# Optimization experiments

Hardware: AMD Instinct MI355X
Metric: run time of the kernel (lower is better)

## Reference

```python
import jax, jax.numpy as jnp
import numpy as np

N, T, H, W, C = 64, 32, 64, 64, 256
HID, NB, P, OUT = 512, 12, 7, 388
CIN = P * P + 2  # 49 patch values + 2 normalized coords


def _ln(x, s):
    # haiku LayerNorm(axis=-1, create_scale=True, create_offset=False), eps=1e-5
    m = jnp.mean(x, axis=-1, keepdims=True)
    v = jnp.var(x, axis=-1, keepdims=True)
    return (x - m) * jax.lax.rsqrt(v + 1e-5) * s


def _dwconv(x, w, b, groups):
    # hk.DepthwiseConv1D, NWC, stride 1, SAME padding; w: [K, 1, C_out]
    y = jax.lax.conv_general_dilated(
        x, w, (1,), 'SAME', dimension_numbers=('NWC', 'WIO', 'NWC'),
        feature_group_count=groups)
    return y + b


def _forward(feature_grid, query_feats, pos, in_w, in_b, dw1_w, dw1_b, dw2_w,
             dw2_b, ln1_s, ln2_s, up_w, up_b, down_w, down_b, lnf_s, out_w,
             out_b):
    pad = P - 1
    # cost volume: einsum('bnc,bthwc->tbnhw') with batch=1, laid out [N,T,H,W]
    corrs = jnp.einsum('nc,thwc->nthw', query_feats, feature_grid)
    padded = jnp.pad(corrs, ((0, 0), (0, 0), (pad, pad), (pad, pad)))
    # extract_patch_depthwise_conv: the separable bilinear bump kernel convolved
    # VALID over the padded map equals a bilinear sample at (o + pos + P/2 - 1).
    pp = pos + P / 2.0 - 1.0  # [N,T,2] (y,x)
    iy = jnp.floor(pp[..., 0])
    ix = jnp.floor(pp[..., 1])
    fy = (pp[..., 0] - iy)[..., None, None]
    fx = (pp[..., 1] - ix)[..., None, None]
    offs = jnp.arange(P, dtype=jnp.int32)
    y0 = iy.astype(jnp.int32)[..., None] + offs  # [N,T,P]
    x0 = ix.astype(jnp.int32)[..., None] + offs  # [N,T,P]
    gat = jax.vmap(jax.vmap(lambda img, yi, xi: img[yi][:, xi]))
    patch = ((1 - fy) * (1 - fx) * gat(padded, y0, x0)
             + (1 - fy) * fx * gat(padded, y0, x0 + 1)
             + fy * (1 - fx) * gat(padded, y0 + 1, x0)
             + fy * fx * gat(padded, y0 + 1, x0 + 1))  # [N,T,P,P]
    x = jnp.concatenate(
        [patch.reshape(patch.shape[0], patch.shape[1], P * P),
         pos / jnp.float32(H)], axis=-1)  # [N,T,CIN]
    # PIPSMLPMixer
    x = x @ in_w + in_b  # [N,T,HID]
    for i in range(NB):
        # PIPsConvBlock: depthwise_conv_residual
        skip = x
        h = _ln(x, ln1_s[i])
        h = jax.nn.gelu(_dwconv(h, dw1_w[i], dw1_b[i], HID))  # ch mult 4
        h = _dwconv(h, dw2_w[i], dw2_b[i], HID * 4)           # ch mult 1
        h = h[..., 0::4] + h[..., 1::4] + h[..., 2::4] + h[..., 3::4]
        x = h + skip
        # conv_channels_mixer
        skip = x
        h = _ln(x, ln2_s[i])
        h = jax.nn.gelu(h @ up_w[i] + up_b[i]) @ down_w[i] + down_b[i]
        x = h + skip
    x = _ln(x, lnf_s)
    return x @ out_w + out_b  # [N,T,OUT]


def setup_inputs() -> dict:
    key = jax.random.key(0)
    ks = jax.random.split(key, 12)
    s = 0.02
    return dict(
        feature_grid=jax.random.normal(ks[0], (T, H, W, C), jnp.float32),
        query_feats=jax.random.normal(ks[1], (N, C), jnp.float32),
        pos=jax.random.uniform(ks[2], (N, T, 2), jnp.float32) * (H - 8),
        in_w=jax.random.normal(ks[3], (CIN, HID), jnp.float32) * s,
        in_b=jnp.zeros((HID,), jnp.float32),
        dw1_w=jax.random.normal(ks[4], (NB, 3, 1, HID * 4), jnp.float32) * s,
        dw1_b=jnp.zeros((NB, HID * 4), jnp.float32),
        dw2_w=jax.random.normal(ks[5], (NB, 3, 1, HID * 4), jnp.float32) * s,
        dw2_b=jnp.zeros((NB, HID * 4), jnp.float32),
        ln1_s=jnp.ones((NB, HID), jnp.float32),
        ln2_s=jnp.ones((NB, HID), jnp.float32),
        up_w=jax.random.normal(ks[6], (NB, HID, HID * 4), jnp.float32) * s,
        up_b=jnp.zeros((NB, HID * 4), jnp.float32),
        down_w=jax.random.normal(ks[7], (NB, HID * 4, HID), jnp.float32) * s,
        down_b=jnp.zeros((NB, HID), jnp.float32),
        lnf_s=jnp.ones((HID,), jnp.float32),
        out_w=jax.random.normal(ks[8], (HID, OUT), jnp.float32) * s,
        out_b=jnp.zeros((OUT,), jnp.float32),
    )


def reference(feature_grid, query_feats, pos, in_w, in_b, dw1_w, dw1_b, dw2_w,
              dw2_b, ln1_s, ln2_s, up_w, up_b, down_w, down_b, lnf_s, out_w,
              out_b):
    return _forward(feature_grid, query_feats, pos, in_w, in_b, dw1_w, dw1_b,
                    dw2_w, dw2_b, ln1_s, ln2_s, up_w, up_b, down_w, down_b,
                    lnf_s, out_w, out_b)
```

## Files before the change

kernel.cpp:

```cpp
#include <hip/hip_runtime.h>
#include <hip/hip_bf16.h>

#define N_    64
#define T_    32
#define H_    64
#define W_    64
#define C_    256
#define HID   512
#define HID4  2048
#define NBLK  12
#define P_    7
#define OUT_  388
#define OUTP  448
#define CIN   51
#define M_    (N_*T_)

typedef __attribute__((ext_vector_type(4))) float f32x4;
typedef __attribute__((ext_vector_type(8))) short bf16x8;

__device__ __forceinline__ float gelu_f(float x) {
    float x3 = x * x * x;
    return 0.5f * x * (1.f + tanhf(0.7978845608028654f * (x + 0.044715f * x3)));
}

__device__ __forceinline__ void gload_lds16(const void* g, void* l) {
    __builtin_amdgcn_global_load_lds(
        (const __attribute__((address_space(1))) void*)g,
        (__attribute__((address_space(3))) void*)l, 16, 0, 0);
}

__global__ __launch_bounds__(256) void patch_kernel(
    const float* __restrict__ fg, const float* __restrict__ qf,
    const float* __restrict__ pos, const float* __restrict__ in_w,
    const float* __restrict__ in_b, float* __restrict__ x) {
    __shared__ float4 q[64];
    __shared__ float g[8][8];
    __shared__ float xrow[CIN];
    int m = blockIdx.x;
    int n = m >> 5;
    int t = m & (T_ - 1);
    int tid = threadIdx.x, wid = tid >> 6, lane = tid & 63;
    if (tid < 64) q[tid] = *(const float4*)&qf[n * C_ + tid * 4];
    __syncthreads();
    float posy = pos[m * 2 + 0];
    float posx = pos[m * 2 + 1];
    float py = posy + 2.5f;
    float px = posx + 2.5f;
    int iy = (int)floorf(py), ix = (int)floorf(px);
    float fy = py - (float)iy, fx = px - (float)ix;
    float4 qv = q[lane];
    #pragma unroll
    for (int i = 0; i < 16; ++i) {
        int idx = wid * 16 + i;
        int a = idx >> 3, b = idx & 7;
        int y = iy + a - 6, xc = ix + b - 6;
        float partial = 0.f;
        if (y >= 0 && y < H_ && xc >= 0 && xc < W_) {
            const float4* fp = (const float4*)&fg[(((t * H_ + y) * W_) + xc) * C_];
            float4 v = fp[lane];
            partial = v.x * qv.x + v.y * qv.y + v.z * qv.z + v.w * qv.w;
        }
        #pragma unroll
        for (int o2 = 32; o2; o2 >>= 1) partial += __shfl_xor(partial, o2);
        if (lane == 0) g[a][b] = partial;
    }
    __syncthreads();
    if (tid < 49) {
        int p = tid / 7, qq = tid % 7;
        xrow[tid] = (1.f - fy) * (1.f - fx) * g[p][qq]
                  + (1.f - fy) * fx         * g[p][qq + 1]
                  + fy         * (1.f - fx) * g[p + 1][qq]
                  + fy         * fx         * g[p + 1][qq + 1];
    } else if (tid == 49) {
        xrow[49] = posy * (1.f / 64.f);
    } else if (tid == 50) {
        xrow[50] = posx * (1.f / 64.f);
    }
    __syncthreads();
    float acc0 = in_b[tid], acc1 = in_b[tid + 256];
    #pragma unroll
    for (int c = 0; c < CIN; ++c) {
        float rv = xrow[c];
        acc0 += rv * in_w[c * HID + tid];
        acc1 += rv * in_w[c * HID + tid + 256];
    }
    x[m * HID + tid] = acc0;
    x[m * HID + tid + 256] = acc1;
}

__global__ __launch_bounds__(512) void fused_dw_kernel(
    const float* __restrict__ xin, float* __restrict__ xout,
    __hip_bfloat16* __restrict__ t1b,
    const float* __restrict__ ln1s, const float* __restrict__ ln2s,
    const float* __restrict__ w1, const float* __restrict__ b1,
    const float* __restrict__ w2, const float* __restrict__ b2) {
    __shared__ float2 part[12][8];
    int n = blockIdx.y;
    int t0 = blockIdx.x * 8;
    int j = threadIdx.x;
    int lane = j & 63, wave = j >> 6;

    float xv[12];
    #pragma unroll
    for (int tt = 0; tt < 12; ++tt) {
        int t = t0 - 2 + tt;
        xv[tt] = (t >= 0 && t < T_) ? xin[(n * T_ + t) * HID + j] : 0.f;
    }
    #pragma unroll
    for (int tt = 0; tt < 12; ++tt) {
        float s = xv[tt], q = xv[tt] * xv[tt];
        #pragma unroll
        for (int o = 32; o; o >>= 1) { s += __shfl_xor(s, o); q += __shfl_xor(q, o); }
        if (lane == 0) part[tt][wave] = make_float2(s, q);
    }
    __syncthreads();
    float s1v = ln1s[j];
    float xl[12];
    #pragma unroll
    for (int tt = 0; tt < 12; ++tt) {
        int t = t0 - 2 + tt;
        if (t >= 0 && t < T_) {
            float s = 0.f, q = 0.f;
            #pragma unroll
            for (int w = 0; w < 8; ++w) { float2 p = part[tt][w]; s += p.x; q += p.y; }
            float mean = s * (1.f / HID);
            float var  = q * (1.f / HID) - mean * mean;
            xl[tt] = (xv[tt] - mean) * rsqrtf(var + 1e-5f) * s1v;
        } else xl[tt] = 0.f;
    }
    float w1a[12], w2a[12], b1a[4];
    #pragma unroll
    for (int r = 0; r < 3; ++r) {
        *(float4*)&w1a[r * 4] = *(const float4*)&w1[r * HID4 + 4 * j];
        *(float4*)&w2a[r * 4] = *(const float4*)&w2[r * HID4 + 4 * j];
    }
    *(float4*)&b1a[0] = *(const float4*)&b1[4 * j];
    float4 b2v = *(const float4*)&b2[4 * j];
    float h[8];
    float b2sum = b2v.x + b2v.y + b2v.z + b2v.w;
    #pragma unroll
    for (int i = 0; i < 8; ++i) h[i] = b2sum;
    #pragma unroll
    for (int k = 0; k < 4; ++k) {
        float gk[10];
        #pragma unroll
        for (int idx = 0; idx < 10; ++idx) {
            int tp = t0 - 1 + idx;
            if (tp >= 0 && tp < T_) {
                float a = b1a[k] + w1a[0 * 4 + k] * xl[idx]
                                 + w1a[1 * 4 + k] * xl[idx + 1]
                                 + w1a[2 * 4 + k] * xl[idx + 2];
                gk[idx] = gelu_f(a);
            } else gk[idx] = 0.f;
        }
        #pragma unroll
        for (int i = 0; i < 8; ++i)
            h[i] += w2a[0 * 4 + k] * gk[i] + w2a[1 * 4 + k] * gk[i + 1]
                  + w2a[2 * 4 + k] * gk[i + 2];
    }
    float xn[8];
    #pragma unroll
    for (int i = 0; i < 8; ++i) xn[i] = xv[i + 2] + h[i];
    __syncthreads();
    #pragma unroll
    for (int i = 0; i < 8; ++i) {
        float s = xn[i], q = xn[i] * xn[i];
        #pragma unroll
        for (int o = 32; o; o >>= 1) { s += __shfl_xor(s, o); q += __shfl_xor(q, o); }
        if (lane == 0) part[i][wave] = make_float2(s, q);
    }
    __syncthreads();
    float s2v = ln2s[j];
    #pragma unroll
    for (int i = 0; i < 8; ++i) {
        float s = 0.f, q = 0.f;
        #pragma unroll
        for (int w = 0; w < 8; ++w) { float2 p = part[i][w]; s += p.x; q += p.y; }
        float mean = s * (1.f / HID);
        float var  = q * (1.f / HID) - mean * mean;
        float rstd = rsqrtf(var + 1e-5f);
        int m = (n * T_ + t0 + i) * HID + j;
        xout[m] = xn[i];
        t1b[m] = __float2bfloat16((xn[i] - mean) * rstd * s2v);
    }
}

__global__ __launch_bounds__(256) void ln_kernel(
    const float* __restrict__ in, const float* __restrict__ s,
    __hip_bfloat16* __restrict__ outb) {
    int wid = threadIdx.x >> 6, lane = threadIdx.x & 63;
    int row = blockIdx.x * 4 + wid;
    const float* r = in + row * HID + lane * 8;
    float4 v0 = *(const float4*)r;
    float4 v1 = *(const float4*)(r + 4);
    float sum = v0.x + v0.y + v0.z + v0.w + v1.x + v1.y + v1.z + v1.w;
    float sq  = v0.x*v0.x + v0.y*v0.y + v0.z*v0.z + v0.w*v0.w
              + v1.x*v1.x + v1.y*v1.y + v1.z*v1.z + v1.w*v1.w;
    #pragma unroll
    for (int o = 32; o; o >>= 1) { sum += __shfl_xor(sum, o); sq += __shfl_xor(sq, o); }
    float mean = sum * (1.f / HID);
    float var  = sq * (1.f / HID) - mean * mean;
    float rstd = rsqrtf(var + 1e-5f);
    const float* sp = s + lane * 8;
    float4 s0 = *(const float4*)sp;
    float4 s1 = *(const float4*)(sp + 4);
    float o[8];
    o[0] = (v0.x - mean) * rstd * s0.x; o[1] = (v0.y - mean) * rstd * s0.y;
    o[2] = (v0.z - mean) * rstd * s0.z; o[3] = (v0.w - mean) * rstd * s0.w;
    o[4] = (v1.x - mean) * rstd * s1.x; o[5] = (v1.y - mean) * rstd * s1.y;
    o[6] = (v1.z - mean) * rstd * s1.z; o[7] = (v1.w - mean) * rstd * s1.w;
    alignas(16) __hip_bfloat16 tmp[8];
    #pragma unroll
    for (int i = 0; i < 8; ++i) tmp[i] = __float2bfloat16(o[i]);
    *(bf16x8*)&outb[row * HID + lane * 8] = *(bf16x8*)tmp;
}

__global__ __launch_bounds__(256) void tcvt_kernel(
    const float* __restrict__ src, __hip_bfloat16* __restrict__ dst,
    int R, int C, int Cpad) {
    __shared__ float tile[32][33];
    size_t zb = blockIdx.z;
    src += zb * (size_t)R * C;
    dst += zb * (size_t)Cpad * R;
    int c0 = blockIdx.x * 32, r0 = blockIdx.y * 32;
    int tx = threadIdx.x & 31, ty = threadIdx.x >> 5;
    #pragma unroll
    for (int i = 0; i < 4; ++i) {
        int r = r0 + ty + i * 8, c = c0 + tx;
        tile[ty + i * 8][tx] = (c < C) ? src[(size_t)r * C + c] : 0.f;
    }
    __syncthreads();
    #pragma unroll
    for (int i = 0; i < 4; ++i) {
        int c = c0 + ty + i * 8, r = r0 + tx;
        dst[(size_t)c * R + r] = __float2bfloat16(tile[tx][ty + i * 8]);
    }
}

template <int KG, int EPI>
__global__ __launch_bounds__(256 * KG) void gemm64(
    const __hip_bfloat16* __restrict__ A, const __hip_bfloat16* __restrict__ Bt,
    const float* __restrict__ bias, float* __restrict__ Cf,
    __hip_bfloat16* __restrict__ Cb, int K, int ldN, int Nstore) {
    __shared__ alignas(16) __hip_bfloat16 As[KG][2][64 * 64];
    __shared__ alignas(16) __hip_bfloat16 Bs[KG][2][64 * 64];
    int tid = threadIdx.x;
    int lane = tid & 63, wave = tid >> 6;
    int g = wave >> 2;
    int w4 = wave & 3;
    int wr = w4 >> 1, wc = w4 & 1;
    int row0 = blockIdx.y * 64, col0 = blockIdx.x * 64;
    int Kg = K / KG;
    int kbase = g * Kg;

    f32x4 acc[2][2];
    #pragma unroll
    for (int m = 0; m < 2; ++m)
        #pragma unroll
        for (int n = 0; n < 2; ++n)
            acc[m][n] = (f32x4){0.f, 0.f, 0.f, 0.f};

    int rI = lane >> 3;
    int cp = lane & 7;

    auto stage = [&](int buf, int k0) {
        #pragma unroll
        for (int s = 0; s < 2; ++s) {
            int rbase = w4 * 16 + s * 8;
            int row = rbase + rI;
            int corig = cp ^ (row & 7);
            gload_lds16(A + (size_t)(row0 + row) * K + kbase + k0 + corig * 8,
                        (char*)As[g][buf] + rbase * 128);
        }
        #pragma unroll
        for (int s = 0; s < 2; ++s) {
            int rbase = w4 * 16 + s * 8;
            int row = rbase + rI;
            int corig = cp ^ (row & 7);
            gload_lds16(Bt + (size_t)(col0 + row) * K + kbase + k0 + corig * 8,
                        (char*)Bs[g][buf] + rbase * 128);
        }
    };

    int nsteps = Kg >> 6;
    stage(0, 0);
    for (int step = 0; step < nsteps; ++step) {
        int cur = step & 1;
        __builtin_amdgcn_s_barrier();
        if (step + 1 < nsteps) {
            stage(cur ^ 1, (step + 1) * 64);
            asm volatile("s_waitcnt vmcnt(4)" ::: "memory");
        } else {
            asm volatile("s_waitcnt vmcnt(0)" ::: "memory");
        }
        __builtin_amdgcn_sched_barrier(0);
        __builtin_amdgcn_s_barrier();
        __builtin_amdgcn_sched_barrier(0);
        #pragma unroll
        for (int kk = 0; kk < 2; ++kk) {
            bf16x8 af[2], bfr[2];
            #pragma unroll
            for (int m = 0; m < 2; ++m) {
                int row = wr * 32 + m * 16 + (lane & 15);
                int chunk = (kk * 4 + (lane >> 4)) ^ (row & 7);
                af[m] = *(const bf16x8*)((const char*)As[g][cur] + row * 128 + chunk * 16);
            }
            #pragma unroll
            for (int n = 0; n < 2; ++n) {
                int row = wc * 32 + n * 16 + (lane & 15);
                int chunk = (kk * 4 + (lane >> 4)) ^ (row & 7);
                bfr[n] = *(const bf16x8*)((const char*)Bs[g][cur] + row * 128 + chunk * 16);
            }
            __builtin_amdgcn_s_setprio(1);
            #pragma unroll
            for (int m = 0; m < 2; ++m)
                #pragma unroll
                for (int n = 0; n < 2; ++n)
                    acc[m][n] = __builtin_amdgcn_mfma_f32_16x16x32_bf16(
                        af[m], bfr[n], acc[m][n], 0, 0, 0);
            __builtin_amdgcn_s_setprio(0);
        }
    }

    int cr = (lane >> 4) * 4;
    int cc = lane & 15;

    if (KG == 2) {
        float* scratch = (float*)&As[0][0][0];
        __syncthreads();
        if (g == 1) {
            #pragma unroll
            for (int m = 0; m < 2; ++m)
                #pragma unroll
                for (int n = 0; n < 2; ++n)
                    #pragma unroll
                    for (int j = 0; j < 4; ++j)
                        scratch[(wr * 32 + m * 16 + cr + j) * 64 +
                                wc * 32 + n * 16 + cc] = acc[m][n][j];
        }
        __syncthreads();
        if (g == 1) return;
        #pragma unroll
        for (int m = 0; m < 2; ++m)
            #pragma unroll
            for (int n = 0; n < 2; ++n)
                #pragma unroll
                for (int j = 0; j < 4; ++j)
                    acc[m][n][j] += scratch[(wr * 32 + m * 16 + cr + j) * 64 +
                                            wc * 32 + n * 16 + cc];
    }

    #pragma unroll
    for (int m = 0; m < 2; ++m) {
        #pragma unroll
        for (int n = 0; n < 2; ++n) {
            #pragma unroll
            for (int j = 0; j < 4; ++j) {
                int row = row0 + wr * 32 + m * 16 + cr + j;
                int col = col0 + wc * 32 + n * 16 + cc;
                float v = acc[m][n][j];
                if (EPI == 0) {
                    if (col < Nstore)
                        Cf[(size_t)row * Nstore + col] = v + bias[col];
                } else if (EPI == 1) {
                    v = gelu_f(v + bias[col]);
                    Cb[(size_t)row * ldN + col] = __float2bfloat16(v);
                } else {
                    Cf[(size_t)row * ldN + col] += v + bias[col];
                }
            }
        }
    }
}

extern "C" void kernel_launch(void* const* d_in, const int* in_sizes, int n_in,
                              void* d_out, int out_size, void* d_ws, size_t ws_size,
                              hipStream_t stream) {
    const float* fg     = (const float*)d_in[0];
    const float* qf     = (const float*)d_in[1];
    const float* pos    = (const float*)d_in[2];
    const float* in_w   = (const float*)d_in[3];
    const float* in_b   = (const float*)d_in[4];
    const float* dw1_w  = (const float*)d_in[5];
    const float* dw1_b  = (const float*)d_in[6];
    const float* dw2_w  = (const float*)d_in[7];
    const float* dw2_b  = (const float*)d_in[8];
    const float* ln1_s  = (const float*)d_in[9];
    const float* ln2_s  = (const float*)d_in[10];
    const float* up_w   = (const float*)d_in[11];
    const float* up_b   = (const float*)d_in[12];
    const float* down_w = (const float*)d_in[13];
    const float* down_b = (const float*)d_in[14];
    const float* lnf_s  = (const float*)d_in[15];
    const float* out_w  = (const float*)d_in[16];
    const float* out_b  = (const float*)d_in[17];
    float* out = (float*)d_out;

    char* ws = (char*)d_ws;
    float* xa = (float*)ws;                        ws += (size_t)M_ * HID * 4;
    float* xb = (float*)ws;                        ws += (size_t)M_ * HID * 4;
    __hip_bfloat16* t1b = (__hip_bfloat16*)ws;     ws += (size_t)M_ * HID * 2;
    __hip_bfloat16* t2b = (__hip_bfloat16*)ws;     ws += (size_t)M_ * HID4 * 2;
    __hip_bfloat16* upT  = (__hip_bfloat16*)ws;    ws += (size_t)NBLK * HID4 * HID * 2;
    __hip_bfloat16* dnT  = (__hip_bfloat16*)ws;    ws += (size_t)NBLK * HID * HID4 * 2;
    __hip_bfloat16* outT = (__hip_bfloat16*)ws;    ws += (size_t)OUTP * HID * 2;

    tcvt_kernel<<<dim3(HID4 / 32, HID / 32, NBLK), 256, 0, stream>>>(
        up_w, upT, HID, HID4, HID4);
    tcvt_kernel<<<dim3(HID / 32, HID4 / 32, NBLK), 256, 0, stream>>>(
        down_w, dnT, HID4, HID, HID);
    tcvt_kernel<<<dim3(OUTP / 32, HID / 32, 1), 256, 0, stream>>>(
        out_w, outT, HID, OUT_, OUTP);

    patch_kernel<<<M_, 256, 0, stream>>>(fg, qf, pos, in_w, in_b, xa);

    float* xc = xa;
    float* xn = xb;
    for (int b = 0; b < NBLK; ++b) {
        fused_dw_kernel<<<dim3(4, N_), 512, 0, stream>>>(
            xc, xn, t1b, ln1_s + b * HID, ln2_s + b * HID,
            dw1_w + b * 3 * HID4, dw1_b + b * HID4,
            dw2_w + b * 3 * HID4, dw2_b + b * HID4);
        gemm64<1, 1><<<dim3(HID4 / 64, M_ / 64), 256, 0, stream>>>(
            t1b, upT + (size_t)b * HID4 * HID, up_b + b * HID4, nullptr, t2b,
            HID, HID4, HID4);
        gemm64<2, 2><<<dim3(HID / 64, M_ / 64), 512, 0, stream>>>(
            t2b, dnT + (size_t)b * HID * HID4, down_b + b * HID, xn, nullptr,
            HID4, HID, HID);
        float* tmp = xc; xc = xn; xn = tmp;
    }

    ln_kernel<<<M_ / 4, 256, 0, stream>>>(xc, lnf_s, t1b);
    gemm64<1, 0><<<dim3(OUTP / 64, M_ / 64), 256, 0, stream>>>(
        t1b, outT, out_b, out, nullptr, HID, OUT_, OUT_);
}
```

Before: 640.3 us.

## Template GEMM tile sizes, use 128x128 tiles for up-projection, add block swizzle

Generalizes the GEMM kernel over block tile and per-wave fragment counts, then launches the up-projection with 128x128 tiles and the output projection with 128x64 tiles. Larger tiles raise MFMA work per shared-memory load and cut global reloads of A and B. The kernel also remaps block IDs in strides of eight to change scheduling order and cache locality. The risk is fewer workgroups: the up GEMM drops to 256 blocks, which may underfill the 256-CU device, and the larger register footprint could lower occupancy.

```diff
diff --git a/kernel.cpp b/kernel.cpp
--- a/kernel.cpp
+++ b/kernel.cpp
@@ -237,27 +237,35 @@
     }
 }
 
-template <int KG, int EPI>
-__global__ __launch_bounds__(256 * KG) void gemm64(
+template <int BM, int BN, int FM, int FN, int KG, int EPI>
+__global__ __launch_bounds__(256 * KG) void gemm_tile(
     const __hip_bfloat16* __restrict__ A, const __hip_bfloat16* __restrict__ Bt,
     const float* __restrict__ bias, float* __restrict__ Cf,
     __hip_bfloat16* __restrict__ Cb, int K, int ldN, int Nstore) {
-    __shared__ alignas(16) __hip_bfloat16 As[KG][2][64 * 64];
-    __shared__ alignas(16) __hip_bfloat16 Bs[KG][2][64 * 64];
+    constexpr int LOADS = (BM + BN) / 32;
+    __shared__ alignas(16) __hip_bfloat16 As[KG][2][BM * 64];
+    __shared__ alignas(16) __hip_bfloat16 Bs[KG][2][BN * 64];
     int tid = threadIdx.x;
     int lane = tid & 63, wave = tid >> 6;
     int g = wave >> 2;
     int w4 = wave & 3;
     int wr = w4 >> 1, wc = w4 & 1;
-    int row0 = blockIdx.y * 64, col0 = blockIdx.x * 64;
+
+    int gx = gridDim.x;
+    int nwg = gx * gridDim.y;
+    int bid = blockIdx.y * gx + blockIdx.x;
+    int cpx = nwg >> 3;
+    int wg = (bid & 7) * cpx + (bid >> 3);
+    int row0 = (wg / gx) * BM, col0 = (wg % gx) * BN;
+
     int Kg = K / KG;
     int kbase = g * Kg;
 
-    f32x4 acc[2][2];
-    #pragma unroll
-    for (int m = 0; m < 2; ++m)
-        #pragma unroll
-        for (int n = 0; n < 2; ++n)
+    f32x4 acc[FM][FN];
+    #pragma unroll
+    for (int m = 0; m < FM; ++m)
+        #pragma unroll
+        for (int n = 0; n < FN; ++n)
             acc[m][n] = (f32x4){0.f, 0.f, 0.f, 0.f};
 
     int rI = lane >> 3;
@@ -265,16 +273,16 @@
 
     auto stage = [&](int buf, int k0) {
         #pragma unroll
-        for (int s = 0; s < 2; ++s) {
-            int rbase = w4 * 16 + s * 8;
+        for (int s = 0; s < BM / 32; ++s) {
+            int rbase = w4 * (BM / 4) + s * 8;
             int row = rbase + rI;
             int corig = cp ^ (row & 7);
             gload_lds16(A + (size_t)(row0 + row) * K + kbase + k0 + corig * 8,
                         (char*)As[g][buf] + rbase * 128);
         }
         #pragma unroll
-        for (int s = 0; s < 2; ++s) {
-            int rbase = w4 * 16 + s * 8;
+        for (int s = 0; s < BN / 32; ++s) {
+            int rbase = w4 * (BN / 4) + s * 8;
             int row = rbase + rI;
             int corig = cp ^ (row & 7);
             gload_lds16(Bt + (size_t)(col0 + row) * K + kbase + k0 + corig * 8,
@@ -289,7 +297,7 @@
         __builtin_amdgcn_s_barrier();
         if (step + 1 < nsteps) {
             stage(cur ^ 1, (step + 1) * 64);
-            asm volatile("s_waitcnt vmcnt(4)" ::: "memory");
+            asm volatile("s_waitcnt vmcnt(%0)" :: "n"(LOADS) : "memory");
         } else {
             asm volatile("s_waitcnt vmcnt(0)" ::: "memory");
         }
@@ -298,24 +306,24 @@
         __builtin_amdgcn_sched_barrier(0);
         #pragma unroll
         for (int kk = 0; kk < 2; ++kk) {
-            bf16x8 af[2], bfr[2];
-            #pragma unroll
-            for (int m = 0; m < 2; ++m) {
-                int row = wr * 32 + m * 16 + (lane & 15);
+            bf16x8 af[FM], bfr[FN];
+            #pragma unroll
+            for (int m = 0; m < FM; ++m) {
+                int row = wr * FM * 16 + m * 16 + (lane & 15);
                 int chunk = (kk * 4 + (lane >> 4)) ^ (row & 7);
                 af[m] = *(const bf16x8*)((const char*)As[g][cur] + row * 128 + chunk * 16);
             }
             #pragma unroll
-            for (int n = 0; n < 2; ++n) {
-                int row = wc * 32 + n * 16 + (lane & 15);
+            for (int n = 0; n < FN; ++n) {
+                int row = wc * FN * 16 + n * 16 + (lane & 15);
                 int chunk = (kk * 4 + (lane >> 4)) ^ (row & 7);
                 bfr[n] = *(const bf16x8*)((const char*)Bs[g][cur] + row * 128 + chunk * 16);
             }
             __builtin_amdgcn_s_setprio(1);
             #pragma unroll
-            for (int m = 0; m < 2; ++m)
+            for (int m = 0; m < FM; ++m)
                 #pragma unroll
-                for (int n = 0; n < 2; ++n)
+                for (int n = 0; n < FN; ++n)
                     acc[m][n] = __builtin_amdgcn_mfma_f32_16x16x32_bf16(
                         af[m], bfr[n], acc[m][n], 0, 0, 0);
             __builtin_amdgcn_s_setprio(0);
@@ -330,34 +338,34 @@
         __syncthreads();
         if (g == 1) {
             #pragma unroll
-            for (int m = 0; m < 2; ++m)
+            for (int m = 0; m < FM; ++m)
                 #pragma unroll
-                for (int n = 0; n < 2; ++n)
+                for (int n = 0; n < FN; ++n)
                     #pragma unroll
                     for (int j = 0; j < 4; ++j)
-                        scratch[(wr * 32 + m * 16 + cr + j) * 64 +
-                                wc * 32 + n * 16 + cc] = acc[m][n][j];
+                        scratch[(wr * FM * 16 + m * 16 + cr + j) * BN +
+                                wc * FN * 16 + n * 16 + cc] = acc[m][n][j];
         }
         __syncthreads();
         if (g == 1) return;
         #pragma unroll
-        for (int m = 0; m < 2; ++m)
-            #pragma unroll
-            for (int n = 0; n < 2; ++n)
+        for (int m = 0; m < FM; ++m)
+            #pragma unroll
+            for (int n = 0; n < FN; ++n)
                 #pragma unroll
                 for (int j = 0; j < 4; ++j)
-                    acc[m][n][j] += scratch[(wr * 32 + m * 16 + cr + j) * 64 +
-                                            wc * 32 + n * 16 + cc];
-    }
-
-    #pragma unroll
-    for (int m = 0; m < 2; ++m) {
-        #pragma unroll
-        for (int n = 0; n < 2; ++n) {
+                    acc[m][n][j] += scratch[(wr * FM * 16 + m * 16 + cr + j) * BN +
+                                            wc * FN * 16 + n * 16 + cc];
+    }
+
+    #pragma unroll
+    for (int m = 0; m < FM; ++m) {
+        #pragma unroll
+        for (int n = 0; n < FN; ++n) {
             #pragma unroll
             for (int j = 0; j < 4; ++j) {
-                int row = row0 + wr * 32 + m * 16 + cr + j;
-                int col = col0 + wc * 32 + n * 16 + cc;
+                int row = row0 + wr * FM * 16 + m * 16 + cr + j;
+                int col = col0 + wc * FN * 16 + n * 16 + cc;
                 float v = acc[m][n][j];
                 if (EPI == 0) {
                     if (col < Nstore)
@@ -421,16 +429,16 @@
             xc, xn, t1b, ln1_s + b * HID, ln2_s + b * HID,
             dw1_w + b * 3 * HID4, dw1_b + b * HID4,
             dw2_w + b * 3 * HID4, dw2_b + b * HID4);
-        gemm64<1, 1><<<dim3(HID4 / 64, M_ / 64), 256, 0, stream>>>(
+        gemm_tile<128, 128, 4, 4, 1, 1><<<dim3(HID4 / 128, M_ / 128), 256, 0, stream>>>(
             t1b, upT + (size_t)b * HID4 * HID, up_b + b * HID4, nullptr, t2b,
             HID, HID4, HID4);
-        gemm64<2, 2><<<dim3(HID / 64, M_ / 64), 512, 0, stream>>>(
+        gemm_tile<64, 64, 2, 2, 2, 2><<<dim3(HID / 64, M_ / 64), 512, 0, stream>>>(
             t2b, dnT + (size_t)b * HID * HID4, down_b + b * HID, xn, nullptr,
             HID4, HID, HID);
         float* tmp = xc; xc = xn; xn = tmp;
     }
 
     ln_kernel<<<M_ / 4, 256, 0, stream>>>(xc, lnf_s, t1b);
-    gemm64<1, 0><<<dim3(OUTP / 64, M_ / 64), 256, 0, stream>>>(
+    gemm_tile<128, 64, 4, 2, 1, 0><<<dim3(OUTP / 64, M_ / 128), 256, 0, stream>>>(
         t1b, outT, out_b, out, nullptr, HID, OUT_, OUT_);
 }
```

Result: slower. 695.9 us (+8.7%).

## Hold A operand in registers for K=512 GEMMs with MFMA-friendly transposed layout

Applied to the files above, without the earlier changes.

The LN outputs are now written in a chunked-transposed bf16 layout (8-element column groups by row) so each wave can load its 16 A rows for the whole K=512 directly into registers. A new gemm_regA kernel stages only B through LDS, with each wave computing a 16x64 tile, and is used for the up-projection and final output GEMMs. The up and down GEMMs also get an XCD-aware block swizzle to improve L2 locality. The cost is 16 extra bf16x8 registers per thread and scattered 2-byte stores from fused_dw_kernel into the transposed layout, which may be poorly coalesced.

```diff
diff --git a/kernel.cpp b/kernel.cpp
--- a/kernel.cpp
+++ b/kernel.cpp
@@ -90,7 +90,7 @@
 
 __global__ __launch_bounds__(512) void fused_dw_kernel(
     const float* __restrict__ xin, float* __restrict__ xout,
-    __hip_bfloat16* __restrict__ t1b,
+    __hip_bfloat16* __restrict__ t1T,
     const float* __restrict__ ln1s, const float* __restrict__ ln2s,
     const float* __restrict__ w1, const float* __restrict__ b1,
     const float* __restrict__ w2, const float* __restrict__ b2) {
@@ -171,6 +171,7 @@
     }
     __syncthreads();
     float s2v = ln2s[j];
+    int cbase = j >> 3, csub = j & 7;
     #pragma unroll
     for (int i = 0; i < 8; ++i) {
         float s = 0.f, q = 0.f;
@@ -179,15 +180,16 @@
         float mean = s * (1.f / HID);
         float var  = q * (1.f / HID) - mean * mean;
         float rstd = rsqrtf(var + 1e-5f);
-        int m = (n * T_ + t0 + i) * HID + j;
-        xout[m] = xn[i];
-        t1b[m] = __float2bfloat16((xn[i] - mean) * rstd * s2v);
+        int row = n * T_ + t0 + i;
+        xout[row * HID + j] = xn[i];
+        t1T[((size_t)cbase * M_ + row) * 8 + csub] =
+            __float2bfloat16((xn[i] - mean) * rstd * s2v);
     }
 }
 
 __global__ __launch_bounds__(256) void ln_kernel(
     const float* __restrict__ in, const float* __restrict__ s,
-    __hip_bfloat16* __restrict__ outb) {
+    __hip_bfloat16* __restrict__ t1T) {
     int wid = threadIdx.x >> 6, lane = threadIdx.x & 63;
     int row = blockIdx.x * 4 + wid;
     const float* r = in + row * HID + lane * 8;
@@ -212,7 +214,7 @@
     alignas(16) __hip_bfloat16 tmp[8];
     #pragma unroll
     for (int i = 0; i < 8; ++i) tmp[i] = __float2bfloat16(o[i]);
-    *(bf16x8*)&outb[row * HID + lane * 8] = *(bf16x8*)tmp;
+    *(bf16x8*)&t1T[((size_t)lane * M_ + row) * 8] = *(bf16x8*)tmp;
 }
 
 __global__ __launch_bounds__(256) void tcvt_kernel(
@@ -237,20 +239,128 @@
     }
 }
 
-template <int KG, int EPI>
-__global__ __launch_bounds__(256 * KG) void gemm64(
+template <int EPI, int SWZ>
+__global__ __launch_bounds__(256, 4) void gemm_regA(
+    const __hip_bfloat16* __restrict__ At,
+    const __hip_bfloat16* __restrict__ Bt,
+    const float* __restrict__ bias, float* __restrict__ Cf,
+    __hip_bfloat16* __restrict__ Cb, int ldN, int Nstore) {
+    constexpr int K = 512;
+    __shared__ alignas(16) __hip_bfloat16 Bs[2][64 * 64];
+    int tid = threadIdx.x;
+    int lane = tid & 63, w = tid >> 6;
+
+    int row0, col0;
+    if (SWZ) {
+        int bid = blockIdx.y * gridDim.x + blockIdx.x;
+        int chunk = gridDim.y >> 3;
+        int xcd = bid & 7;
+        int i = bid >> 3;
+        row0 = (xcd * chunk + (i % chunk)) * 64;
+        col0 = (i / chunk) * 64;
+    } else {
+        row0 = blockIdx.y * 64;
+        col0 = blockIdx.x * 64;
+    }
+
+    int sub = lane >> 4;
+    int arow = row0 + w * 16 + (lane & 15);
+    bf16x8 areg[16];
+    #pragma unroll
+    for (int kb = 0; kb < 16; ++kb) {
+        int c = kb * 4 + sub;
+        areg[kb] = *(const bf16x8*)&At[((size_t)c * M_ + arow) * 8];
+    }
+
+    int rI = lane >> 3;
+    int cp = lane & 7;
+    auto stageB = [&](int buf, int k0) {
+        #pragma unroll
+        for (int s = 0; s < 2; ++s) {
+            int rbase = w * 16 + s * 8;
+            int row = rbase + rI;
+            int corig = cp ^ (row & 7);
+            gload_lds16(Bt + (size_t)(col0 + row) * K + k0 + corig * 8,
+                        (char*)Bs[buf] + rbase * 128);
+        }
+    };
+
+    f32x4 acc[4];
+    #pragma unroll
+    for (int n = 0; n < 4; ++n) acc[n] = (f32x4){0.f, 0.f, 0.f, 0.f};
+
+    stageB(0, 0);
+    #pragma unroll
+    for (int step = 0; step < 8; ++step) {
+        int cur = step & 1;
+        __builtin_amdgcn_s_barrier();
+        if (step < 7) {
+            stageB(cur ^ 1, (step + 1) * 64);
+            asm volatile("s_waitcnt vmcnt(2)" ::: "memory");
+        } else {
+            asm volatile("s_waitcnt vmcnt(0)" ::: "memory");
+        }
+        __builtin_amdgcn_sched_barrier(0);
+        __builtin_amdgcn_s_barrier();
+        __builtin_amdgcn_sched_barrier(0);
+        #pragma unroll
+        for (int kk = 0; kk < 2; ++kk) {
+            bf16x8 bfr[4];
+            #pragma unroll
+            for (int n = 0; n < 4; ++n) {
+                int row = n * 16 + (lane & 15);
+                int chunk = (kk * 4 + sub) ^ (row & 7);
+                bfr[n] = *(const bf16x8*)((const char*)Bs[cur] + row * 128 + chunk * 16);
+            }
+            __builtin_amdgcn_s_setprio(1);
+            #pragma unroll
+            for (int n = 0; n < 4; ++n)
+                acc[n] = __builtin_amdgcn_mfma_f32_16x16x32_bf16(
+                    areg[step * 2 + kk], bfr[n], acc[n], 0, 0, 0);
+            __builtin_amdgcn_s_setprio(0);
+        }
+    }
+
+    int cr = (lane >> 4) * 4;
+    int cc = lane & 15;
+    #pragma unroll
+    for (int n = 0; n < 4; ++n) {
+        #pragma unroll
+        for (int j = 0; j < 4; ++j) {
+            int row = row0 + w * 16 + cr + j;
+            int col = col0 + n * 16 + cc;
+            float v = acc[n][j];
+            if (EPI == 0) {
+                if (col < Nstore)
+                    Cf[(size_t)row * Nstore + col] = v + bias[col];
+            } else {
+                v = gelu_f(v + bias[col]);
+                Cb[(size_t)row * ldN + col] = __float2bfloat16(v);
+            }
+        }
+    }
+}
+
+__global__ __launch_bounds__(512) void gemm_down(
     const __hip_bfloat16* __restrict__ A, const __hip_bfloat16* __restrict__ Bt,
     const float* __restrict__ bias, float* __restrict__ Cf,
-    __hip_bfloat16* __restrict__ Cb, int K, int ldN, int Nstore) {
-    __shared__ alignas(16) __hip_bfloat16 As[KG][2][64 * 64];
-    __shared__ alignas(16) __hip_bfloat16 Bs[KG][2][64 * 64];
+    int K, int ldN) {
+    __shared__ alignas(16) __hip_bfloat16 As[2][2][64 * 64];
+    __shared__ alignas(16) __hip_bfloat16 Bs[2][2][64 * 64];
     int tid = threadIdx.x;
     int lane = tid & 63, wave = tid >> 6;
     int g = wave >> 2;
     int w4 = wave & 3;
     int wr = w4 >> 1, wc = w4 & 1;
-    int row0 = blockIdx.y * 64, col0 = blockIdx.x * 64;
-    int Kg = K / KG;
+
+    int bid = blockIdx.y * gridDim.x + blockIdx.x;
+    int chunk = gridDim.y >> 3;
+    int xcd = bid & 7;
+    int i = bid >> 3;
+    int row0 = (xcd * chunk + (i % chunk)) * 64;
+    int col0 = (i / chunk) * 64;
+
+    int Kg = K / 2;
     int kbase = g * Kg;
 
     f32x4 acc[2][2];
@@ -302,14 +412,14 @@
             #pragma unroll
             for (int m = 0; m < 2; ++m) {
                 int row = wr * 32 + m * 16 + (lane & 15);
-                int chunk = (kk * 4 + (lane >> 4)) ^ (row & 7);
-                af[m] = *(const bf16x8*)((const char*)As[g][cur] + row * 128 + chunk * 16);
+                int chunk2 = (kk * 4 + (lane >> 4)) ^ (row & 7);
+                af[m] = *(const bf16x8*)((const char*)As[g][cur] + row * 128 + chunk2 * 16);
             }
             #pragma unroll
             for (int n = 0; n < 2; ++n) {
                 int row = wc * 32 + n * 16 + (lane & 15);
-                int chunk = (kk * 4 + (lane >> 4)) ^ (row & 7);
-                bfr[n] = *(const bf16x8*)((const char*)Bs[g][cur] + row * 128 + chunk * 16);
+                int chunk2 = (kk * 4 + (lane >> 4)) ^ (row & 7);
+                bfr[n] = *(const bf16x8*)((const char*)Bs[g][cur] + row * 128 + chunk2 * 16);
             }
             __builtin_amdgcn_s_setprio(1);
             #pragma unroll
@@ -325,31 +435,20 @@
     int cr = (lane >> 4) * 4;
     int cc = lane & 15;
 
-    if (KG == 2) {
-        float* scratch = (float*)&As[0][0][0];
-        __syncthreads();
-        if (g == 1) {
-            #pragma unroll
-            for (int m = 0; m < 2; ++m)
-                #pragma unroll
-                for (int n = 0; n < 2; ++n)
-                    #pragma unroll
-                    for (int j = 0; j < 4; ++j)
-                        scratch[(wr * 32 + m * 16 + cr + j) * 64 +
-                                wc * 32 + n * 16 + cc] = acc[m][n][j];
-        }
-        __syncthreads();
-        if (g == 1) return;
+    float* scratch = (float*)&As[0][0][0];
+    __syncthreads();
+    if (g == 1) {
         #pragma unroll
         for (int m = 0; m < 2; ++m)
             #pragma unroll
             for (int n = 0; n < 2; ++n)
                 #pragma unroll
                 for (int j = 0; j < 4; ++j)
-                    acc[m][n][j] += scratch[(wr * 32 + m * 16 + cr + j) * 64 +
-                                            wc * 32 + n * 16 + cc];
-    }
-
+                    scratch[(wr * 32 + m * 16 + cr + j) * 64 +
+                            wc * 32 + n * 16 + cc] = acc[m][n][j];
+    }
+    __syncthreads();
+    if (g == 1) return;
     #pragma unroll
     for (int m = 0; m < 2; ++m) {
         #pragma unroll
@@ -358,16 +457,10 @@
             for (int j = 0; j < 4; ++j) {
                 int row = row0 + wr * 32 + m * 16 + cr + j;
                 int col = col0 + wc * 32 + n * 16 + cc;
-                float v = acc[m][n][j];
-                if (EPI == 0) {
-                    if (col < Nstore)
-                        Cf[(size_t)row * Nstore + col] = v + bias[col];
-                } else if (EPI == 1) {
-                    v = gelu_f(v + bias[col]);
-                    Cb[(size_t)row * ldN + col] = __float2bfloat16(v);
-                } else {
-                    Cf[(size_t)row * ldN + col] += v + bias[col];
-                }
+                float v = acc[m][n][j] +
+                          scratch[(wr * 32 + m * 16 + cr + j) * 64 +
+                                  wc * 32 + n * 16 + cc];
+                Cf[(size_t)row * ldN + col] += v + bias[col];
             }
         }
     }
@@ -399,7 +492,7 @@
     char* ws = (char*)d_ws;
     float* xa = (float*)ws;                        ws += (size_t)M_ * HID * 4;
     float* xb = (float*)ws;                        ws += (size_t)M_ * HID * 4;
-    __hip_bfloat16* t1b = (__hip_bfloat16*)ws;     ws += (size_t)M_ * HID * 2;
+    __hip_bfloat16* t1T = (__hip_bfloat16*)ws;     ws += (size_t)M_ * HID * 2;
     __hip_bfloat16* t2b = (__hip_bfloat16*)ws;     ws += (size_t)M_ * HID4 * 2;
     __hip_bfloat16* upT  = (__hip_bfloat16*)ws;    ws += (size_t)NBLK * HID4 * HID * 2;
     __hip_bfloat16* dnT  = (__hip_bfloat16*)ws;    ws += (size_t)NBLK * HID * HID4 * 2;
@@ -418,19 +511,19 @@
     float* xn = xb;
     for (int b = 0; b < NBLK; ++b) {
         fused_dw_kernel<<<dim3(4, N_), 512, 0, stream>>>(
-            xc, xn, t1b, ln1_s + b * HID, ln2_s + b * HID,
+            xc, xn, t1T, ln1_s + b * HID, ln2_s + b * HID,
             dw1_w + b * 3 * HID4, dw1_b + b * HID4,
             dw2_w + b * 3 * HID4, dw2_b + b * HID4);
-        gemm64<1, 1><<<dim3(HID4 / 64, M_ / 64), 256, 0, stream>>>(
-            t1b, upT + (size_t)b * HID4 * HID, up_b + b * HID4, nullptr, t2b,
-            HID, HID4, HID4);
-        gemm64<2, 2><<<dim3(HID / 64, M_ / 64), 512, 0, stream>>>(
-            t2b, dnT + (size_t)b * HID * HID4, down_b + b * HID, xn, nullptr,
-            HID4, HID, HID);
+        gemm_regA<1, 1><<<dim3(HID4 / 64, M_ / 64), 256, 0, stream>>>(
+            t1T, upT + (size_t)b * HID4 * HID, up_b + b * HID4, nullptr, t2b,
+            HID4, HID4);
+        gemm_down<<<dim3(HID / 64, M_ / 64), 512, 0, stream>>>(
+            t2b, dnT + (size_t)b * HID * HID4, down_b + b * HID, xn,
+            HID4, HID);
         float* tmp = xc; xc = xn; xn = tmp;
     }
 
-    ln_kernel<<<M_ / 4, 256, 0, stream>>>(xc, lnf_s, t1b);
-    gemm64<1, 0><<<dim3(OUTP / 64, M_ / 64), 256, 0, stream>>>(
-        t1b, outT, out_b, out, nullptr, HID, OUT_, OUT_);
-}
+    ln_kernel<<<M_ / 4, 256, 0, stream>>>(xc, lnf_s, t1T);
+    gemm_regA<0, 0><<<dim3(OUTP / 64, M_ / 64), 256, 0, stream>>>(
+        t1T, outT, out_b, out, nullptr, OUT_, OUT_);
+}
```

After: 607.3 us, median of 2. 5.2% less time.
